# Performance work log

Hardware: AMD Instinct MI355X
Metric: run time of the kernel (lower is better)

Reference implementation:

```python
import jax, jax.numpy as jnp
import numpy as np
from jax import lax

TOP_K = 8
EPS = 1e-12


def l2_normalize(x, axis):
    sq = jnp.sum(x * x, axis=axis, keepdims=True)
    return x * lax.rsqrt(jnp.maximum(sq, EPS))


def setup_inputs() -> dict:
    key = jax.random.key(0)
    k1, k2, k3, k4 = jax.random.split(key, 4)
    B, N, C = 256, 197, 768
    POOL, LEN = 1024, 8
    x_embed = jax.random.normal(k1, (B, N, C), dtype=jnp.float32)
    prompt = jax.random.uniform(k2, (POOL, LEN, C), dtype=jnp.float32, minval=-1.0, maxval=1.0)
    prompt_key = jax.random.uniform(k3, (POOL, C), dtype=jnp.float32, minval=-1.0, maxval=1.0)
    # kaiming_normal fan_out: std = sqrt(2 / fan_out)
    proj_w = jax.random.normal(k4, (C, C), dtype=jnp.float32) * np.sqrt(2.0 / C).astype(np.float32)
    proj_b = jnp.zeros((C,), dtype=jnp.float32)
    return {"x_embed": x_embed, "prompt": prompt, "prompt_key": prompt_key,
            "proj_w": proj_w, "proj_b": proj_b}


def reference(x_embed, prompt, prompt_key, proj_w, proj_b):
    B = x_embed.shape[0]
    # embedding_key == 'mean'
    x_mean = jnp.mean(x_embed, axis=1)                     # [B, C]
    prompt_norm = l2_normalize(prompt_key, axis=1)         # [P, C]
    x_norm = l2_normalize(x_mean, axis=1)                  # [B, C]
    similarity = x_norm @ prompt_norm.T                    # [B, P]
    _, idx = lax.top_k(similarity, TOP_K)                  # [B, K]
    # gather prompts: [B, K, L, C] -> [B, K*L, C]
    bp = prompt[idx]
    Bk, K, L, C = bp.shape
    batched_prompt = bp.reshape(Bk, K * L, C)
    # projection + residual (dropout in eval mode = identity)
    batched_prompt = batched_prompt @ proj_w.T + proj_b + batched_prompt
    # key loss term
    batched_key_norm = prompt_norm[idx]                    # [B, K, C]
    reduce_sim = jnp.sum(batched_key_norm * x_norm[:, None, :]) / B
    prompted = jnp.concatenate([x_embed[:, :1, :], batched_prompt, x_embed[:, 1:, :]], axis=1)
    return prompted, reduce_sim
```

## Files before the change

kernel.cpp:

```cpp
#include <hip/hip_runtime.h>
#include <float.h>
#include <math.h>

#define B_    256
#define N_    197
#define C_    768
#define POOL_ 1024
#define LEN_  8
#define TOPK_ 8
#define PROWS (POOL_*LEN_)
#define OUTROWS 261

typedef __attribute__((ext_vector_type(8))) short short8_t;
typedef __attribute__((ext_vector_type(4))) float f32x4;

static const size_t OFF_XMEAN = 0;
static const size_t OFF_XNORM = 786432;
static const size_t OFF_PNORM = 1572864;
static const size_t OFF_SIM   = 4718592;
static const size_t OFF_IDX   = 5767168;
static const size_t OFF_ACC   = 5775360;
static const size_t OFF_ABF   = 5775616;
static const size_t OFF_WBF   = 18358528;
static const size_t OFF_PROJ  = 19538176;

__global__ __launch_bounds__(256) void k1_mean_copy(const float* __restrict__ x,
                                                    float* __restrict__ out,
                                                    float* __restrict__ xmean) {
    int b   = blockIdx.x / 3;
    int seg = blockIdx.x % 3;
    int t = threadIdx.x;
    int r = t >> 6;
    int c = t & 63;
    int c4 = seg * 64 + c;
    const f32x4* xin  = (const f32x4*)x   + (size_t)b * (N_ * 192) + c4;
    f32x4*       outb = (f32x4*)out       + (size_t)b * (OUTROWS * 192) + c4;

    float sx = 0.f, sy = 0.f, sz = 0.f, sw = 0.f;
    #pragma unroll 7
    for (int n = r; n < 196; n += 4) {
        f32x4 v = __builtin_nontemporal_load(&xin[(size_t)n * 192]);
        sx += v.x; sy += v.y; sz += v.z; sw += v.w;
        int orow = (n == 0) ? 0 : (64 + n);
        __builtin_nontemporal_store(v, &outb[(size_t)orow * 192]);
    }
    if (r == 0) {
        f32x4 v = __builtin_nontemporal_load(&xin[(size_t)196 * 192]);
        sx += v.x; sy += v.y; sz += v.z; sw += v.w;
        __builtin_nontemporal_store(v, &outb[(size_t)260 * 192]);
    }
    __shared__ f32x4 red[4][64];
    f32x4 s; s.x = sx; s.y = sy; s.z = sz; s.w = sw;
    red[r][c] = s;
    __syncthreads();
    if (r == 0) {
        f32x4 a = red[0][c], b2 = red[1][c], c2 = red[2][c], d = red[3][c];
        const float inv = 1.0f / (float)N_;
        f32x4 m;
        m.x = (a.x + b2.x + c2.x + d.x) * inv;
        m.y = (a.y + b2.y + c2.y + d.y) * inv;
        m.z = (a.z + b2.z + c2.z + d.z) * inv;
        m.w = (a.w + b2.w + c2.w + d.w) * inv;
        ((f32x4*)xmean)[b * 192 + c4] = m;
    }
}

__device__ __forceinline__ unsigned short f2bf(float f) {
    unsigned int u = __float_as_uint(f);
    u += 0x7fffu + ((u >> 16) & 1u);
    return (unsigned short)(u >> 16);
}
__global__ __launch_bounds__(256) void k2_norm_convert(const float* __restrict__ xmean,
                                                       const float* __restrict__ pkey,
                                                       float* __restrict__ xnorm,
                                                       float* __restrict__ pnorm,
                                                       float* __restrict__ sim_accum,
                                                       const float* __restrict__ prompt,
                                                       const float* __restrict__ projw,
                                                       unsigned short* __restrict__ Abf,
                                                       unsigned short* __restrict__ Wbf) {
    int r = blockIdx.x;
    int t = threadIdx.x;
    if (r < B_ + POOL_) {
        __shared__ float red[256];
        const float* src; float* dst;
        if (r < B_) { src = xmean + (size_t)r * C_; dst = xnorm + (size_t)r * C_; }
        else        { src = pkey  + (size_t)(r - B_) * C_; dst = pnorm + (size_t)(r - B_) * C_; }
        float v0 = src[t], v1 = src[t + 256], v2 = src[t + 512];
        red[t] = v0*v0 + v1*v1 + v2*v2;
        __syncthreads();
        for (int off = 128; off > 0; off >>= 1) {
            if (t < off) red[t] += red[t + off];
            __syncthreads();
        }
        float inv = 1.0f / sqrtf(fmaxf(red[0], 1e-12f));
        dst[t] = v0 * inv; dst[t + 256] = v1 * inv; dst[t + 512] = v2 * inv;
        if (r == 0 && t == 0) sim_accum[0] = 0.0f;
    } else {
        int i4 = (r - (B_ + POOL_)) * 256 + t;
        float4 v; unsigned short* d;
        if (i4 < (PROWS * C_ / 4)) {
            v = ((const float4*)prompt)[i4];
            d = Abf + (size_t)i4 * 4;
        } else {
            int j4 = i4 - PROWS * C_ / 4;
            v = ((const float4*)projw)[j4];
            d = Wbf + (size_t)j4 * 4;
        }
        ushort4 o; o.x = f2bf(v.x); o.y = f2bf(v.y); o.z = f2bf(v.z); o.w = f2bf(v.w);
        *(ushort4*)d = o;
    }
}

__global__ __launch_bounds__(256) void k3_sim(const float* __restrict__ xnorm,
                                              const float* __restrict__ pnorm,
                                              float* __restrict__ sim) {
    __shared__ float As[32][36];
    __shared__ float Bs[32][36];
    int t = threadIdx.x;
    int m0 = blockIdx.y * 32, n0 = blockIdx.x * 32;
    int lrow = t >> 3, lc = (t & 7) * 4;
    int ty = t >> 4, tx = t & 15;
    float a00 = 0.f, a01 = 0.f, a10 = 0.f, a11 = 0.f;
    float4 va = *(const float4*)&xnorm[(size_t)(m0 + lrow) * C_ + lc];
    float4 vb = *(const float4*)&pnorm[(size_t)(n0 + lrow) * C_ + lc];
    for (int k0 = 0; k0 < C_; k0 += 32) {
        __syncthreads();
        *(float4*)&As[lrow][lc] = va;
        *(float4*)&Bs[lrow][lc] = vb;
        __syncthreads();
        if (k0 + 32 < C_) {
            va = *(const float4*)&xnorm[(size_t)(m0 + lrow) * C_ + k0 + 32 + lc];
            vb = *(const float4*)&pnorm[(size_t)(n0 + lrow) * C_ + k0 + 32 + lc];
        }
        #pragma unroll
        for (int kk = 0; kk < 32; kk += 4) {
            float4 A0 = *(const float4*)&As[ty*2][kk];
            float4 A1 = *(const float4*)&As[ty*2+1][kk];
            float4 B0 = *(const float4*)&Bs[tx*2][kk];
            float4 B1 = *(const float4*)&Bs[tx*2+1][kk];
            a00 += A0.x*B0.x; a00 += A0.y*B0.y; a00 += A0.z*B0.z; a00 += A0.w*B0.w;
            a01 += A0.x*B1.x; a01 += A0.y*B1.y; a01 += A0.z*B1.z; a01 += A0.w*B1.w;
            a10 += A1.x*B0.x; a10 += A1.y*B0.y; a10 += A1.z*B0.z; a10 += A1.w*B0.w;
            a11 += A1.x*B1.x; a11 += A1.y*B1.y; a11 += A1.z*B1.z; a11 += A1.w*B1.w;
        }
    }
    sim[(size_t)(m0 + ty*2    ) * POOL_ + n0 + tx*2    ] = a00;
    sim[(size_t)(m0 + ty*2    ) * POOL_ + n0 + tx*2 + 1] = a01;
    sim[(size_t)(m0 + ty*2 + 1) * POOL_ + n0 + tx*2    ] = a10;
    sim[(size_t)(m0 + ty*2 + 1) * POOL_ + n0 + tx*2 + 1] = a11;
}

__global__ __launch_bounds__(256) void k4_topk(const float* __restrict__ sim,
                                               int* __restrict__ idx,
                                               float* __restrict__ sim_accum) {
    __shared__ float vals[POOL_];
    __shared__ float wv[4];
    __shared__ int   wi[4];
    int b = blockIdx.x, t = threadIdx.x;
    int wave = t >> 6;
    #pragma unroll
    for (int i = 0; i < 4; ++i) vals[t + 256*i] = sim[(size_t)b * POOL_ + t + 256*i];
    __syncthreads();
    float sumv = 0.0f;
    for (int k = 0; k < TOPK_; ++k) {
        float bv = -FLT_MAX; int bi = POOL_;
        #pragma unroll
        for (int i = 0; i < 4; ++i) {
            int n = t + 256*i;
            float v = vals[n];
            if (v > bv) { bv = v; bi = n; }
        }
        #pragma unroll
        for (int off = 32; off > 0; off >>= 1) {
            float v2 = __shfl_down(bv, off);
            int   i2 = __shfl_down(bi, off);
            if (v2 > bv || (v2 == bv && i2 < bi)) { bv = v2; bi = i2; }
        }
        if ((t & 63) == 0) { wv[wave] = bv; wi[wave] = bi; }
        __syncthreads();
        if (t == 0) {
            float fv = wv[0]; int fi = wi[0];
            #pragma unroll
            for (int w = 1; w < 4; ++w) {
                float v2 = wv[w]; int i2 = wi[w];
                if (v2 > fv || (v2 == fv && i2 < fi)) { fv = v2; fi = i2; }
            }
            idx[b*TOPK_ + k] = fi;
            sumv += fv;
            vals[fi] = -FLT_MAX;
        }
        __syncthreads();
    }
    if (t == 0) atomicAdd(sim_accum, sumv);
}

__global__ __launch_bounds__(256) void k5_gemm(const unsigned short* __restrict__ A,
                                               const unsigned short* __restrict__ W,
                                               const float* __restrict__ bias,
                                               const float* __restrict__ resid,
                                               float* __restrict__ out) {
    __shared__ short As[2][64*32];
    __shared__ short Bs[2][128*32];
    const int tid = threadIdx.x;
    const int m0 = blockIdx.y * 64, n0 = blockIdx.x * 128;
    const int wave = tid >> 6, lane = tid & 63;
    const int quad = lane >> 4, lr = lane & 15;
    const int srow = tid >> 2;
    const int scol = (tid & 3) * 8;

    f32x4 acc[4][2] = {};

    auto stage = [&](int buf, int kt) {
        const int k0 = kt * 32;
        __builtin_amdgcn_global_load_lds(
            (const __attribute__((address_space(1))) void*)&A[(size_t)(m0 + srow) * C_ + k0 + scol],
            (__attribute__((address_space(3))) void*)&As[buf][srow*32 + scol], 16, 0, 0);
        __builtin_amdgcn_global_load_lds(
            (const __attribute__((address_space(1))) void*)&W[(size_t)(n0 + srow) * C_ + k0 + scol],
            (__attribute__((address_space(3))) void*)&Bs[buf][srow*32 + scol], 16, 0, 0);
        __builtin_amdgcn_global_load_lds(
            (const __attribute__((address_space(1))) void*)&W[(size_t)(n0 + 64 + srow) * C_ + k0 + scol],
            (__attribute__((address_space(3))) void*)&Bs[buf][(64 + srow)*32 + scol], 16, 0, 0);
    };
    auto compute = [&](int buf) {
        short8_t af[4], bf[2];
        #pragma unroll
        for (int i = 0; i < 4; ++i)
            af[i] = *(const short8_t*)&As[buf][(i*16 + lr)*32 + quad*8];
        #pragma unroll
        for (int j = 0; j < 2; ++j)
            bf[j] = *(const short8_t*)&Bs[buf][(wave*32 + j*16 + lr)*32 + quad*8];
        #pragma unroll
        for (int i = 0; i < 4; ++i)
            #pragma unroll
            for (int j = 0; j < 2; ++j)
                acc[i][j] = __builtin_amdgcn_mfma_f32_16x16x32_bf16(af[i], bf[j], acc[i][j], 0, 0, 0);
    };

    stage(0, 0);
    __syncthreads();
    int cur = 0;
    for (int kt = 0; kt < 23; ++kt) {
        stage(cur ^ 1, kt + 1);
        compute(cur);
        __syncthreads();
        cur ^= 1;
    }
    compute(cur);

    #pragma unroll
    for (int j = 0; j < 2; ++j) {
        const int n = n0 + wave*32 + j*16 + lr;
        const float bn = bias[n];
        #pragma unroll
        for (int i = 0; i < 4; ++i) {
            const int mbase = m0 + i*16 + quad*4;
            #pragma unroll
            for (int r = 0; r < 4; ++r) {
                const int m = mbase + r;
                out[(size_t)m * C_ + n] = acc[i][j][r] + bn + resid[(size_t)m * C_ + n];
            }
        }
    }
}

__global__ __launch_bounds__(256) void k6_gather(const float* __restrict__ projall,
                                                 const int* __restrict__ idx,
                                                 const float* __restrict__ sim_accum,
                                                 float* __restrict__ out) {
    int row = blockIdx.x * 4 + (threadIdx.x >> 6);
    int t = threadIdx.x & 63;
    int b = row >> 6, j = row & 63;
    int k = j >> 3, l = j & 7;
    int p = idx[b * TOPK_ + k];
    const f32x4* src = (const f32x4*)projall + (size_t)(p * LEN_ + l) * 192;
    f32x4* dst = (f32x4*)out + (size_t)(b * OUTROWS + 1 + j) * 192;
    __builtin_nontemporal_store(src[t],       &dst[t]);
    __builtin_nontemporal_store(src[t + 64],  &dst[t + 64]);
    __builtin_nontemporal_store(src[t + 128], &dst[t + 128]);
    if (row == 0 && t == 0)
        out[(size_t)B_ * OUTROWS * C_] = sim_accum[0] * (1.0f / (float)B_);
}

extern "C" void kernel_launch(void* const* d_in, const int* in_sizes, int n_in,
                              void* d_out, int out_size, void* d_ws, size_t ws_size,
                              hipStream_t stream) {
    const float* x_embed = (const float*)d_in[0];
    const float* prompt  = (const float*)d_in[1];
    const float* pkey    = (const float*)d_in[2];
    const float* projw   = (const float*)d_in[3];
    const float* projb   = (const float*)d_in[4];
    float* out = (float*)d_out;
    char* ws = (char*)d_ws;

    float*          xmean   = (float*)(ws + OFF_XMEAN);
    float*          xnorm   = (float*)(ws + OFF_XNORM);
    float*          pnorm   = (float*)(ws + OFF_PNORM);
    float*          sim     = (float*)(ws + OFF_SIM);
    int*            idxp    = (int*)(ws + OFF_IDX);
    float*          acc     = (float*)(ws + OFF_ACC);
    unsigned short* Abf     = (unsigned short*)(ws + OFF_ABF);
    unsigned short* Wbf     = (unsigned short*)(ws + OFF_WBF);
    float*          projall = (float*)(ws + OFF_PROJ);

    const int convBlocks = (PROWS * C_ / 4 + 768 * 768 / 4) / 256;
    k1_mean_copy<<<B_ * 3, 256, 0, stream>>>(x_embed, out, xmean);
    k2_norm_convert<<<B_ + POOL_ + convBlocks, 256, 0, stream>>>(xmean, pkey, xnorm, pnorm, acc,
                                                                 prompt, projw, Abf, Wbf);
    k3_sim<<<dim3(POOL_ / 32, B_ / 32), 256, 0, stream>>>(xnorm, pnorm, sim);
    k4_topk<<<B_, 256, 0, stream>>>(sim, idxp, acc);
    k5_gemm<<<dim3(C_ / 128, PROWS / 64), 256, 0, stream>>>(Abf, Wbf, projb, prompt, projall);
    k6_gather<<<B_ * 64 / 4, 256, 0, stream>>>(projall, idxp, acc, out);
}
```

Before: 408.9 us.

## Fuse six kernels into three by merging mean, norm, GEMMs and gather

Cuts the pipeline from six launches to three. The mean/copy, norm-scale computation and bf16 conversion now share one kernel. The similarity GEMM runs in the same launch as the projection GEMM, on the unnormalized inputs, with the inverse norms applied at the end instead of storing normalized copies. Top-k and the prompt gather are also fused, and the final loss is written by the last block using an atomic counter. This removes launch gaps and intermediate normalized buffers, but adds heterogeneous blocks and 768-thread blocks that may lower occupancy.

```diff
diff --git a/kernel.cpp b/kernel.cpp
--- a/kernel.cpp
+++ b/kernel.cpp
@@ -15,89 +15,96 @@
 typedef __attribute__((ext_vector_type(4))) float f32x4;
 
 static const size_t OFF_XMEAN = 0;
-static const size_t OFF_XNORM = 786432;
-static const size_t OFF_PNORM = 1572864;
-static const size_t OFF_SIM   = 4718592;
-static const size_t OFF_IDX   = 5767168;
-static const size_t OFF_ACC   = 5775360;
-static const size_t OFF_ABF   = 5775616;
-static const size_t OFF_WBF   = 18358528;
-static const size_t OFF_PROJ  = 19538176;
-
-__global__ __launch_bounds__(256) void k1_mean_copy(const float* __restrict__ x,
-                                                    float* __restrict__ out,
-                                                    float* __restrict__ xmean) {
-    int b   = blockIdx.x / 3;
-    int seg = blockIdx.x % 3;
-    int t = threadIdx.x;
-    int r = t >> 6;
-    int c = t & 63;
-    int c4 = seg * 64 + c;
-    const f32x4* xin  = (const f32x4*)x   + (size_t)b * (N_ * 192) + c4;
-    f32x4*       outb = (f32x4*)out       + (size_t)b * (OUTROWS * 192) + c4;
-
-    float sx = 0.f, sy = 0.f, sz = 0.f, sw = 0.f;
-    #pragma unroll 7
-    for (int n = r; n < 196; n += 4) {
-        f32x4 v = __builtin_nontemporal_load(&xin[(size_t)n * 192]);
-        sx += v.x; sy += v.y; sz += v.z; sw += v.w;
-        int orow = (n == 0) ? 0 : (64 + n);
-        __builtin_nontemporal_store(v, &outb[(size_t)orow * 192]);
-    }
-    if (r == 0) {
-        f32x4 v = __builtin_nontemporal_load(&xin[(size_t)196 * 192]);
-        sx += v.x; sy += v.y; sz += v.z; sw += v.w;
-        __builtin_nontemporal_store(v, &outb[(size_t)260 * 192]);
-    }
-    __shared__ f32x4 red[4][64];
-    f32x4 s; s.x = sx; s.y = sy; s.z = sz; s.w = sw;
-    red[r][c] = s;
-    __syncthreads();
-    if (r == 0) {
-        f32x4 a = red[0][c], b2 = red[1][c], c2 = red[2][c], d = red[3][c];
-        const float inv = 1.0f / (float)N_;
-        f32x4 m;
-        m.x = (a.x + b2.x + c2.x + d.x) * inv;
-        m.y = (a.y + b2.y + c2.y + d.y) * inv;
-        m.z = (a.z + b2.z + c2.z + d.z) * inv;
-        m.w = (a.w + b2.w + c2.w + d.w) * inv;
-        ((f32x4*)xmean)[b * 192 + c4] = m;
-    }
-}
+static const size_t OFF_INVX  = 786432;
+static const size_t OFF_INVP  = 787456;
+static const size_t OFF_SIM   = 791552;
+static const size_t OFF_ACC   = 1840128;
+static const size_t OFF_ABF   = 1840384;
+static const size_t OFF_WBF   = 14423296;
+static const size_t OFF_PROJ  = 15602944;
 
 __device__ __forceinline__ unsigned short f2bf(float f) {
     unsigned int u = __float_as_uint(f);
     u += 0x7fffu + ((u >> 16) & 1u);
     return (unsigned short)(u >> 16);
 }
-__global__ __launch_bounds__(256) void k2_norm_convert(const float* __restrict__ xmean,
-                                                       const float* __restrict__ pkey,
-                                                       float* __restrict__ xnorm,
-                                                       float* __restrict__ pnorm,
-                                                       float* __restrict__ sim_accum,
-                                                       const float* __restrict__ prompt,
-                                                       const float* __restrict__ projw,
-                                                       unsigned short* __restrict__ Abf,
-                                                       unsigned short* __restrict__ Wbf) {
-    int r = blockIdx.x;
-    int t = threadIdx.x;
-    if (r < B_ + POOL_) {
-        __shared__ float red[256];
-        const float* src; float* dst;
-        if (r < B_) { src = xmean + (size_t)r * C_; dst = xnorm + (size_t)r * C_; }
-        else        { src = pkey  + (size_t)(r - B_) * C_; dst = pnorm + (size_t)(r - B_) * C_; }
-        float v0 = src[t], v1 = src[t + 256], v2 = src[t + 512];
-        red[t] = v0*v0 + v1*v1 + v2*v2;
+
+__global__ __launch_bounds__(768) void kA(const float* __restrict__ x,
+                                          const float* __restrict__ pkey,
+                                          const float* __restrict__ prompt,
+                                          const float* __restrict__ projw,
+                                          float* __restrict__ out,
+                                          float* __restrict__ xmean,
+                                          float* __restrict__ invx,
+                                          float* __restrict__ invp,
+                                          unsigned short* __restrict__ Abf,
+                                          unsigned short* __restrict__ Wbf,
+                                          float* __restrict__ accum) {
+    __shared__ f32x4 red[4][192];
+    __shared__ float sq[256];
+    __shared__ float wsum[12];
+    const int bid = blockIdx.x, t = threadIdx.x;
+
+    if (bid < B_) {
+        const int b = bid;
+        const int r = t / 192;
+        const int c = t - r * 192;
+        const f32x4* xin  = (const f32x4*)x   + (size_t)b * (N_ * 192) + c;
+        f32x4*       outb = (f32x4*)out       + (size_t)b * (OUTROWS * 192) + c;
+        float sx = 0.f, sy = 0.f, sz = 0.f, sw = 0.f;
+        #pragma unroll 7
+        for (int n = r; n < 196; n += 4) {
+            f32x4 v = __builtin_nontemporal_load(&xin[(size_t)n * 192]);
+            sx += v.x; sy += v.y; sz += v.z; sw += v.w;
+            int orow = (n == 0) ? 0 : (64 + n);
+            __builtin_nontemporal_store(v, &outb[(size_t)orow * 192]);
+        }
+        if (r == 0) {
+            f32x4 v = __builtin_nontemporal_load(&xin[(size_t)196 * 192]);
+            sx += v.x; sy += v.y; sz += v.z; sw += v.w;
+            __builtin_nontemporal_store(v, &outb[(size_t)260 * 192]);
+        }
+        f32x4 s; s.x = sx; s.y = sy; s.z = sz; s.w = sw;
+        red[r][c] = s;
+        if (t < 256) sq[t] = 0.f;
+        __syncthreads();
+        if (r == 0) {
+            f32x4 a = red[0][c], b2 = red[1][c], c2 = red[2][c], d = red[3][c];
+            const float inv = 1.0f / (float)N_;
+            f32x4 m;
+            m.x = (a.x + b2.x + c2.x + d.x) * inv;
+            m.y = (a.y + b2.y + c2.y + d.y) * inv;
+            m.z = (a.z + b2.z + c2.z + d.z) * inv;
+            m.w = (a.w + b2.w + c2.w + d.w) * inv;
+            ((f32x4*)xmean)[b * 192 + c] = m;
+            sq[c] = m.x*m.x + m.y*m.y + m.z*m.z + m.w*m.w;
+        }
         __syncthreads();
         for (int off = 128; off > 0; off >>= 1) {
-            if (t < off) red[t] += red[t + off];
+            if (t < off) sq[t] += sq[t + off];
             __syncthreads();
         }
-        float inv = 1.0f / sqrtf(fmaxf(red[0], 1e-12f));
-        dst[t] = v0 * inv; dst[t + 256] = v1 * inv; dst[t + 512] = v2 * inv;
-        if (r == 0 && t == 0) sim_accum[0] = 0.0f;
+        if (t == 0) {
+            invx[b] = 1.0f / sqrtf(fmaxf(sq[0], 1e-12f));
+            if (b == 0) { accum[0] = 0.0f; ((int*)accum)[1] = 0; }
+        }
+    } else if (bid < B_ + POOL_) {
+        const int p = bid - B_;
+        float v = pkey[(size_t)p * C_ + t];
+        float sg = v * v;
+        #pragma unroll
+        for (int off = 32; off > 0; off >>= 1) sg += __shfl_down(sg, off);
+        const int wave = t >> 6;
+        if ((t & 63) == 0) wsum[wave] = sg;
+        __syncthreads();
+        if (t == 0) {
+            float tot = wsum[0];
+            #pragma unroll
+            for (int w = 1; w < 12; ++w) tot += wsum[w];
+            invp[p] = 1.0f / sqrtf(fmaxf(tot, 1e-12f));
+        }
     } else {
-        int i4 = (r - (B_ + POOL_)) * 256 + t;
+        int i4 = (bid - (B_ + POOL_)) * 768 + t;
         float4 v; unsigned short* d;
         if (i4 < (PROWS * C_ / 4)) {
             v = ((const float4*)prompt)[i4];
@@ -112,53 +119,133 @@
     }
 }
 
-__global__ __launch_bounds__(256) void k3_sim(const float* __restrict__ xnorm,
-                                              const float* __restrict__ pnorm,
-                                              float* __restrict__ sim) {
-    __shared__ float As[32][36];
-    __shared__ float Bs[32][36];
-    int t = threadIdx.x;
-    int m0 = blockIdx.y * 32, n0 = blockIdx.x * 32;
-    int lrow = t >> 3, lc = (t & 7) * 4;
-    int ty = t >> 4, tx = t & 15;
-    float a00 = 0.f, a01 = 0.f, a10 = 0.f, a11 = 0.f;
-    float4 va = *(const float4*)&xnorm[(size_t)(m0 + lrow) * C_ + lc];
-    float4 vb = *(const float4*)&pnorm[(size_t)(n0 + lrow) * C_ + lc];
-    for (int k0 = 0; k0 < C_; k0 += 32) {
-        __syncthreads();
-        *(float4*)&As[lrow][lc] = va;
-        *(float4*)&Bs[lrow][lc] = vb;
-        __syncthreads();
-        if (k0 + 32 < C_) {
-            va = *(const float4*)&xnorm[(size_t)(m0 + lrow) * C_ + k0 + 32 + lc];
-            vb = *(const float4*)&pnorm[(size_t)(n0 + lrow) * C_ + k0 + 32 + lc];
-        }
+__global__ __launch_bounds__(256) void kB(const unsigned short* __restrict__ A,
+                                          const unsigned short* __restrict__ W,
+                                          const float* __restrict__ bias,
+                                          const float* __restrict__ resid,
+                                          float* __restrict__ projout,
+                                          const float* __restrict__ xmean,
+                                          const float* __restrict__ pkey,
+                                          const float* __restrict__ invx,
+                                          const float* __restrict__ invp,
+                                          float* __restrict__ sim) {
+    __shared__ short As5[2][64*32];
+    __shared__ short Bs5[2][128*32];
+    __shared__ float As3[32][36];
+    __shared__ float Bs3[32][36];
+    const int tid = threadIdx.x;
+    const int bid = blockIdx.x;
+
+    if (bid < 768) {
+        const int m0 = (bid / 6) * 64, n0 = (bid % 6) * 128;
+        const int wave = tid >> 6, lane = tid & 63;
+        const int quad = lane >> 4, lr = lane & 15;
+        const int srow = tid >> 2;
+        const int scol = (tid & 3) * 8;
+
+        f32x4 acc[4][2] = {};
+
+        auto stage = [&](int buf, int kt) {
+            const int k0 = kt * 32;
+            __builtin_amdgcn_global_load_lds(
+                (const __attribute__((address_space(1))) void*)&A[(size_t)(m0 + srow) * C_ + k0 + scol],
+                (__attribute__((address_space(3))) void*)&As5[buf][srow*32 + scol], 16, 0, 0);
+            __builtin_amdgcn_global_load_lds(
+                (const __attribute__((address_space(1))) void*)&W[(size_t)(n0 + srow) * C_ + k0 + scol],
+                (__attribute__((address_space(3))) void*)&Bs5[buf][srow*32 + scol], 16, 0, 0);
+            __builtin_amdgcn_global_load_lds(
+                (const __attribute__((address_space(1))) void*)&W[(size_t)(n0 + 64 + srow) * C_ + k0 + scol],
+                (__attribute__((address_space(3))) void*)&Bs5[buf][(64 + srow)*32 + scol], 16, 0, 0);
+        };
+        auto compute = [&](int buf) {
+            short8_t af[4], bf[2];
+            #pragma unroll
+            for (int i = 0; i < 4; ++i)
+                af[i] = *(const short8_t*)&As5[buf][(i*16 + lr)*32 + quad*8];
+            #pragma unroll
+            for (int j = 0; j < 2; ++j)
+                bf[j] = *(const short8_t*)&Bs5[buf][(wave*32 + j*16 + lr)*32 + quad*8];
+            #pragma unroll
+            for (int i = 0; i < 4; ++i)
+                #pragma unroll
+                for (int j = 0; j < 2; ++j)
+                    acc[i][j] = __builtin_amdgcn_mfma_f32_16x16x32_bf16(af[i], bf[j], acc[i][j], 0, 0, 0);
+        };
+
+        stage(0, 0);
+        __syncthreads();
+        int cur = 0;
+        for (int kt = 0; kt < 23; ++kt) {
+            stage(cur ^ 1, kt + 1);
+            compute(cur);
+            __syncthreads();
+            cur ^= 1;
+        }
+        compute(cur);
+
         #pragma unroll
-        for (int kk = 0; kk < 32; kk += 4) {
-            float4 A0 = *(const float4*)&As[ty*2][kk];
-            float4 A1 = *(const float4*)&As[ty*2+1][kk];
-            float4 B0 = *(const float4*)&Bs[tx*2][kk];
-            float4 B1 = *(const float4*)&Bs[tx*2+1][kk];
-            a00 += A0.x*B0.x; a00 += A0.y*B0.y; a00 += A0.z*B0.z; a00 += A0.w*B0.w;
-            a01 += A0.x*B1.x; a01 += A0.y*B1.y; a01 += A0.z*B1.z; a01 += A0.w*B1.w;
-            a10 += A1.x*B0.x; a10 += A1.y*B0.y; a10 += A1.z*B0.z; a10 += A1.w*B0.w;
-            a11 += A1.x*B1.x; a11 += A1.y*B1.y; a11 += A1.z*B1.z; a11 += A1.w*B1.w;
-        }
-    }
-    sim[(size_t)(m0 + ty*2    ) * POOL_ + n0 + tx*2    ] = a00;
-    sim[(size_t)(m0 + ty*2    ) * POOL_ + n0 + tx*2 + 1] = a01;
-    sim[(size_t)(m0 + ty*2 + 1) * POOL_ + n0 + tx*2    ] = a10;
-    sim[(size_t)(m0 + ty*2 + 1) * POOL_ + n0 + tx*2 + 1] = a11;
-}
-
-__global__ __launch_bounds__(256) void k4_topk(const float* __restrict__ sim,
-                                               int* __restrict__ idx,
-                                               float* __restrict__ sim_accum) {
+        for (int j = 0; j < 2; ++j) {
+            const int n = n0 + wave*32 + j*16 + lr;
+            const float bn = bias[n];
+            #pragma unroll
+            for (int i = 0; i < 4; ++i) {
+                const int mbase = m0 + i*16 + quad*4;
+                #pragma unroll
+                for (int r = 0; r < 4; ++r) {
+                    const int m = mbase + r;
+                    projout[(size_t)m * C_ + n] = acc[i][j][r] + bn + resid[(size_t)m * C_ + n];
+                }
+            }
+        }
+    } else {
+        const int q = bid - 768;
+        const int m0 = (q >> 5) * 32, n0 = (q & 31) * 32;
+        const int t = tid;
+        const int lrow = t >> 3, lc = (t & 7) * 4;
+        const int ty = t >> 4, tx = t & 15;
+        float a00 = 0.f, a01 = 0.f, a10 = 0.f, a11 = 0.f;
+        float4 va = *(const float4*)&xmean[(size_t)(m0 + lrow) * C_ + lc];
+        float4 vb = *(const float4*)&pkey [(size_t)(n0 + lrow) * C_ + lc];
+        for (int k0 = 0; k0 < C_; k0 += 32) {
+            __syncthreads();
+            *(float4*)&As3[lrow][lc] = va;
+            *(float4*)&Bs3[lrow][lc] = vb;
+            __syncthreads();
+            if (k0 + 32 < C_) {
+                va = *(const float4*)&xmean[(size_t)(m0 + lrow) * C_ + k0 + 32 + lc];
+                vb = *(const float4*)&pkey [(size_t)(n0 + lrow) * C_ + k0 + 32 + lc];
+            }
+            #pragma unroll
+            for (int kk = 0; kk < 32; kk += 4) {
+                float4 A0 = *(const float4*)&As3[ty*2][kk];
+                float4 A1 = *(const float4*)&As3[ty*2+1][kk];
+                float4 B0 = *(const float4*)&Bs3[tx*2][kk];
+                float4 B1 = *(const float4*)&Bs3[tx*2+1][kk];
+                a00 += A0.x*B0.x; a00 += A0.y*B0.y; a00 += A0.z*B0.z; a00 += A0.w*B0.w;
+                a01 += A0.x*B1.x; a01 += A0.y*B1.y; a01 += A0.z*B1.z; a01 += A0.w*B1.w;
+                a10 += A1.x*B0.x; a10 += A1.y*B0.y; a10 += A1.z*B0.z; a10 += A1.w*B0.w;
+                a11 += A1.x*B1.x; a11 += A1.y*B1.y; a11 += A1.z*B1.z; a11 += A1.w*B1.w;
+            }
+        }
+        const float im0 = invx[m0 + ty*2], im1 = invx[m0 + ty*2 + 1];
+        const float ip0 = invp[n0 + tx*2], ip1 = invp[n0 + tx*2 + 1];
+        sim[(size_t)(m0 + ty*2    ) * POOL_ + n0 + tx*2    ] = a00 * im0 * ip0;
+        sim[(size_t)(m0 + ty*2    ) * POOL_ + n0 + tx*2 + 1] = a01 * im0 * ip1;
+        sim[(size_t)(m0 + ty*2 + 1) * POOL_ + n0 + tx*2    ] = a10 * im1 * ip0;
+        sim[(size_t)(m0 + ty*2 + 1) * POOL_ + n0 + tx*2 + 1] = a11 * im1 * ip1;
+    }
+}
+
+__global__ __launch_bounds__(256) void kC(const float* __restrict__ sim,
+                                          const float* __restrict__ projall,
+                                          float* __restrict__ accum,
+                                          float* __restrict__ out) {
     __shared__ float vals[POOL_];
     __shared__ float wv[4];
     __shared__ int   wi[4];
-    int b = blockIdx.x, t = threadIdx.x;
-    int wave = t >> 6;
+    __shared__ int   sidx[TOPK_];
+    const int b = blockIdx.x, t = threadIdx.x;
+    const int wave = t >> 6, lane = t & 63;
     #pragma unroll
     for (int i = 0; i < 4; ++i) vals[t + 256*i] = sim[(size_t)b * POOL_ + t + 256*i];
     __syncthreads();
@@ -177,7 +264,7 @@
             int   i2 = __shfl_down(bi, off);
             if (v2 > bv || (v2 == bv && i2 < bi)) { bv = v2; bi = i2; }
         }
-        if ((t & 63) == 0) { wv[wave] = bv; wi[wave] = bi; }
+        if (lane == 0) { wv[wave] = bv; wi[wave] = bi; }
         __syncthreads();
         if (t == 0) {
             float fv = wv[0]; int fi = wi[0];
@@ -186,101 +273,32 @@
                 float v2 = wv[w]; int i2 = wi[w];
                 if (v2 > fv || (v2 == fv && i2 < fi)) { fv = v2; fi = i2; }
             }
-            idx[b*TOPK_ + k] = fi;
+            sidx[k] = fi;
             sumv += fv;
             vals[fi] = -FLT_MAX;
         }
         __syncthreads();
     }
-    if (t == 0) atomicAdd(sim_accum, sumv);
-}
-
-__global__ __launch_bounds__(256) void k5_gemm(const unsigned short* __restrict__ A,
-                                               const unsigned short* __restrict__ W,
-                                               const float* __restrict__ bias,
-                                               const float* __restrict__ resid,
-                                               float* __restrict__ out) {
-    __shared__ short As[2][64*32];
-    __shared__ short Bs[2][128*32];
-    const int tid = threadIdx.x;
-    const int m0 = blockIdx.y * 64, n0 = blockIdx.x * 128;
-    const int wave = tid >> 6, lane = tid & 63;
-    const int quad = lane >> 4, lr = lane & 15;
-    const int srow = tid >> 2;
-    const int scol = (tid & 3) * 8;
-
-    f32x4 acc[4][2] = {};
-
-    auto stage = [&](int buf, int kt) {
-        const int k0 = kt * 32;
-        __builtin_amdgcn_global_load_lds(
-            (const __attribute__((address_space(1))) void*)&A[(size_t)(m0 + srow) * C_ + k0 + scol],
-            (__attribute__((address_space(3))) void*)&As[buf][srow*32 + scol], 16, 0, 0);
-        __builtin_amdgcn_global_load_lds(
-            (const __attribute__((address_space(1))) void*)&W[(size_t)(n0 + srow) * C_ + k0 + scol],
-            (__attribute__((address_space(3))) void*)&Bs[buf][srow*32 + scol], 16, 0, 0);
-        __builtin_amdgcn_global_load_lds(
-            (const __attribute__((address_space(1))) void*)&W[(size_t)(n0 + 64 + srow) * C_ + k0 + scol],
-            (__attribute__((address_space(3))) void*)&Bs[buf][(64 + srow)*32 + scol], 16, 0, 0);
-    };
-    auto compute = [&](int buf) {
-        short8_t af[4], bf[2];
-        #pragma unroll
-        for (int i = 0; i < 4; ++i)
-            af[i] = *(const short8_t*)&As[buf][(i*16 + lr)*32 + quad*8];
-        #pragma unroll
-        for (int j = 0; j < 2; ++j)
-            bf[j] = *(const short8_t*)&Bs[buf][(wave*32 + j*16 + lr)*32 + quad*8];
-        #pragma unroll
-        for (int i = 0; i < 4; ++i)
-            #pragma unroll
-            for (int j = 0; j < 2; ++j)
-                acc[i][j] = __builtin_amdgcn_mfma_f32_16x16x32_bf16(af[i], bf[j], acc[i][j], 0, 0, 0);
-    };
-
-    stage(0, 0);
-    __syncthreads();
-    int cur = 0;
-    for (int kt = 0; kt < 23; ++kt) {
-        stage(cur ^ 1, kt + 1);
-        compute(cur);
-        __syncthreads();
-        cur ^= 1;
-    }
-    compute(cur);
-
-    #pragma unroll
-    for (int j = 0; j < 2; ++j) {
-        const int n = n0 + wave*32 + j*16 + lr;
-        const float bn = bias[n];
-        #pragma unroll
-        for (int i = 0; i < 4; ++i) {
-            const int mbase = m0 + i*16 + quad*4;
-            #pragma unroll
-            for (int r = 0; r < 4; ++r) {
-                const int m = mbase + r;
-                out[(size_t)m * C_ + n] = acc[i][j][r] + bn + resid[(size_t)m * C_ + n];
-            }
-        }
-    }
-}
-
-__global__ __launch_bounds__(256) void k6_gather(const float* __restrict__ projall,
-                                                 const int* __restrict__ idx,
-                                                 const float* __restrict__ sim_accum,
-                                                 float* __restrict__ out) {
-    int row = blockIdx.x * 4 + (threadIdx.x >> 6);
-    int t = threadIdx.x & 63;
-    int b = row >> 6, j = row & 63;
-    int k = j >> 3, l = j & 7;
-    int p = idx[b * TOPK_ + k];
-    const f32x4* src = (const f32x4*)projall + (size_t)(p * LEN_ + l) * 192;
-    f32x4* dst = (f32x4*)out + (size_t)(b * OUTROWS + 1 + j) * 192;
-    __builtin_nontemporal_store(src[t],       &dst[t]);
-    __builtin_nontemporal_store(src[t + 64],  &dst[t + 64]);
-    __builtin_nontemporal_store(src[t + 128], &dst[t + 128]);
-    if (row == 0 && t == 0)
-        out[(size_t)B_ * OUTROWS * C_] = sim_accum[0] * (1.0f / (float)B_);
+    #pragma unroll 4
+    for (int jj = 0; jj < 16; ++jj) {
+        const int j = wave * 16 + jj;
+        const int p = sidx[j >> 3];
+        const int l = j & 7;
+        const f32x4* src = (const f32x4*)projall + (size_t)(p * LEN_ + l) * 192;
+        f32x4* dst = (f32x4*)out + (size_t)(b * OUTROWS + 1 + j) * 192;
+        __builtin_nontemporal_store(src[lane],       &dst[lane]);
+        __builtin_nontemporal_store(src[lane + 64],  &dst[lane + 64]);
+        __builtin_nontemporal_store(src[lane + 128], &dst[lane + 128]);
+    }
+    if (t == 0) {
+        atomicAdd(&accum[0], sumv);
+        __threadfence();
+        int done = atomicAdd((int*)accum + 1, 1);
+        if (done == B_ - 1) {
+            float tot = atomicAdd(&accum[0], 0.0f);
+            out[(size_t)B_ * OUTROWS * C_] = tot * (1.0f / (float)B_);
+        }
+    }
 }
 
 extern "C" void kernel_launch(void* const* d_in, const int* in_sizes, int n_in,
@@ -295,21 +313,18 @@
     char* ws = (char*)d_ws;
 
     float*          xmean   = (float*)(ws + OFF_XMEAN);
-    float*          xnorm   = (float*)(ws + OFF_XNORM);
-    float*          pnorm   = (float*)(ws + OFF_PNORM);
+    float*          invx    = (float*)(ws + OFF_INVX);
+    float*          invp    = (float*)(ws + OFF_INVP);
     float*          sim     = (float*)(ws + OFF_SIM);
-    int*            idxp    = (int*)(ws + OFF_IDX);
     float*          acc     = (float*)(ws + OFF_ACC);
     unsigned short* Abf     = (unsigned short*)(ws + OFF_ABF);
     unsigned short* Wbf     = (unsigned short*)(ws + OFF_WBF);
     float*          projall = (float*)(ws + OFF_PROJ);
 
-    const int convBlocks = (PROWS * C_ / 4 + 768 * 768 / 4) / 256;
-    k1_mean_copy<<<B_ * 3, 256, 0, stream>>>(x_embed, out, xmean);
-    k2_norm_convert<<<B_ + POOL_ + convBlocks, 256, 0, stream>>>(xmean, pkey, xnorm, pnorm, acc,
-                                                                 prompt, projw, Abf, Wbf);
-    k3_sim<<<dim3(POOL_ / 32, B_ / 32), 256, 0, stream>>>(xnorm, pnorm, sim);
-    k4_topk<<<B_, 256, 0, stream>>>(sim, idxp, acc);
-    k5_gemm<<<dim3(C_ / 128, PROWS / 64), 256, 0, stream>>>(Abf, Wbf, projb, prompt, projall);
-    k6_gather<<<B_ * 64 / 4, 256, 0, stream>>>(projall, idxp, acc, out);
-}
+    const int convBlocks = (PROWS * C_ / 4 + 768 * 768 / 4) / 768;
+    kA<<<B_ + POOL_ + convBlocks, 768, 0, stream>>>(x_embed, pkey, prompt, projw,
+                                                    out, xmean, invx, invp, Abf, Wbf, acc);
+    kB<<<1024, 256, 0, stream>>>(Abf, Wbf, projb, prompt, projall,
+                                 xmean, pkey, invx, invp, sim);
+    kC<<<B_, 256, 0, stream>>>(sim, projall, acc, out);
+}
```

After: 423.8 us. 3.6% more time.
